# Kernel optimization log

Hardware: AMD Instinct MI355X
Metric: run time of the kernel (lower is better)

The kernel has to match this reference:

```python
import jax, jax.numpy as jnp
import numpy as np

EPS = 1e-12
SHRINK = 0.0025

def _l2norm(x, axis=1):
    return x / jnp.maximum(jnp.linalg.norm(x, axis=axis, keepdims=True), EPS)

def setup_inputs() -> dict:
    key = jax.random.key(0)
    ks = jax.random.split(key, 6)
    N, C, H, W = 32, 512, 32, 32
    mem_dim, spatial = 512, H * W
    hid = spatial // 2
    x = jax.random.normal(ks[0], (N, C, H, W), dtype=jnp.float32)
    memory = jax.random.normal(ks[1], (mem_dim, spatial), dtype=jnp.float32)
    memory = _l2norm(memory, axis=1)  # buffer is L2-normalized at init
    w1 = jax.random.normal(ks[2], (hid, spatial), dtype=jnp.float32) * 0.02
    b1 = jax.random.normal(ks[3], (hid,), dtype=jnp.float32) * 0.02
    w2 = jax.random.normal(ks[4], (spatial, hid), dtype=jnp.float32) * 0.02
    b2 = jax.random.normal(ks[5], (spatial,), dtype=jnp.float32) * 0.02
    return {"x": x, "memory": memory, "w1": w1, "b1": b1, "w2": w2, "b2": b2}

def reference(x, memory, w1, b1, w2, b2):
    N, C, H, W = x.shape
    mem_dim = memory.shape[0]
    input_flat = x.reshape(N * C, H * W)
    input_norm = _l2norm(input_flat, axis=1)
    # shared MLP over memory bank: Linear -> ReLU -> Linear -> ReLU
    h = jax.nn.relu(memory @ w1.T + b1)
    mem_proc = jax.nn.relu(h @ w2.T + b2)
    memory_norm = _l2norm(mem_proc, axis=1)
    # addressing: cosine sim -> softmax -> hard shrink -> L1 renorm
    att = jax.nn.softmax(input_norm @ memory_norm.T, axis=1)  # [N*C, M]
    att = jax.nn.relu(att - SHRINK)
    att = att / jnp.maximum(att.sum(axis=1, keepdims=True), EPS)  # p=1 norm (att >= 0)
    output = (att @ memory_norm).reshape(N, C, H, W)
    att_channel_avg = att.reshape(N, C, mem_dim).mean(axis=1)  # [N, M]
    att_spatial = jnp.broadcast_to(att_channel_avg[:, :, None, None], (N, mem_dim, H, W))
    return output, att_spatial, input_flat, memory_norm, att
```

## Files before the change

### kernel.cpp

```cpp
#include <hip/hip_runtime.h>

typedef float  f32x4  __attribute__((ext_vector_type(4)));
typedef __bf16 bf16x8 __attribute__((ext_vector_type(8)));
typedef __bf16 bf16x4 __attribute__((ext_vector_type(4)));

#define L2EPS   1e-12f
#define SHRINKC 0.0025f


__device__ __forceinline__ bf16x8 pack_bf16(f32x4 v0, f32x4 v1) {
  bf16x8 r;
  r[0] = (__bf16)v0[0]; r[1] = (__bf16)v0[1]; r[2] = (__bf16)v0[2]; r[3] = (__bf16)v0[3];
  r[4] = (__bf16)v1[0]; r[5] = (__bf16)v1[1]; r[6] = (__bf16)v1[2]; r[7] = (__bf16)v1[3];
  return r;
}

__device__ __forceinline__ bf16x8 load_cvt_bf16x8(const float* p) {
  const f32x4* q = (const f32x4*)p;
  return pack_bf16(q[0], q[1]);
}

__global__ __launch_bounds__(256) void rownorm_copy(
    const float* __restrict__ x, float* __restrict__ out_flat,
    float* __restrict__ invnorm) {
  const int r = blockIdx.x;
  const int tid = threadIdx.x;
  const f32x4 v = *(const f32x4*)(x + (size_t)r * 1024 + tid * 4);
  *(f32x4*)(out_flat + (size_t)r * 1024 + tid * 4) = v;
  float ss = v[0]*v[0] + v[1]*v[1] + v[2]*v[2] + v[3]*v[3];
  #pragma unroll
  for (int d = 1; d < 64; d <<= 1) ss += __shfl_xor(ss, d);
  __shared__ float wsum[4];
  if ((tid & 63) == 0) wsum[tid >> 6] = ss;
  __syncthreads();
  if (tid == 0) {
    float t = wsum[0] + wsum[1] + wsum[2] + wsum[3];
    invnorm[r] = 1.f / fmaxf(sqrtf(t), L2EPS);
  }
}

__global__ __launch_bounds__(256) void gemm_bt_bias_relu(
    const float* __restrict__ A, const float* __restrict__ B,
    const float* __restrict__ bias, float* __restrict__ C,
    int M, int N, int K) {
  const int r0   = blockIdx.x * 32;
  const int wave = threadIdx.x >> 6;
  const int lane = threadIdx.x & 63;
  const int quad = lane >> 4;
  const int m    = lane & 15;
  const int n0   = blockIdx.y * 128 + wave * 32;

  f32x4 acc[2][2] = {};
  for (int k0 = 0; k0 < K; k0 += 32) {
    const int kk = k0 + quad * 8;
    bf16x8 a[2], b[2];
    #pragma unroll
    for (int rg = 0; rg < 2; ++rg)
      a[rg] = load_cvt_bf16x8(A + (size_t)(r0 + rg * 16 + m) * K + kk);
    #pragma unroll
    for (int cf = 0; cf < 2; ++cf)
      b[cf] = load_cvt_bf16x8(B + (size_t)(n0 + cf * 16 + m) * K + kk);
    #pragma unroll
    for (int rg = 0; rg < 2; ++rg)
      #pragma unroll
      for (int cf = 0; cf < 2; ++cf)
        acc[rg][cf] = __builtin_amdgcn_mfma_f32_16x16x32_bf16(a[rg], b[cf], acc[rg][cf], 0, 0, 0);
  }
  #pragma unroll
  for (int rg = 0; rg < 2; ++rg)
    #pragma unroll
    for (int cf = 0; cf < 2; ++cf) {
      const int n = n0 + cf * 16 + m;
      const float bv = bias[n];
      #pragma unroll
      for (int vi = 0; vi < 4; ++vi) {
        const int r = r0 + rg * 16 + quad * 4 + vi;
        C[(size_t)r * N + n] = fmaxf(acc[rg][cf][vi] + bv, 0.f);
      }
    }
}

__global__ __launch_bounds__(256) void norm_rows(
    const float* __restrict__ mp, float* __restrict__ mn_f32,
    __bf16* __restrict__ mn_bf16) {
  const int r = blockIdx.x;
  const int tid = threadIdx.x;
  const f32x4 v = *(const f32x4*)(mp + (size_t)r * 1024 + tid * 4);
  float ss = v[0]*v[0] + v[1]*v[1] + v[2]*v[2] + v[3]*v[3];
  #pragma unroll
  for (int d = 1; d < 64; d <<= 1) ss += __shfl_xor(ss, d);
  __shared__ float wsum[4];
  __shared__ float invs;
  if ((tid & 63) == 0) wsum[tid >> 6] = ss;
  __syncthreads();
  if (tid == 0) {
    float t = wsum[0] + wsum[1] + wsum[2] + wsum[3];
    invs = 1.f / fmaxf(sqrtf(t), L2EPS);
  }
  __syncthreads();
  const float iv = invs;
  f32x4 o = v * iv;
  *(f32x4*)(mn_f32 + (size_t)r * 1024 + tid * 4) = o;
  bf16x4 ob;
  ob[0] = (__bf16)o[0]; ob[1] = (__bf16)o[1]; ob[2] = (__bf16)o[2]; ob[3] = (__bf16)o[3];
  *(bf16x4*)(mn_bf16 + (size_t)r * 1024 + tid * 4) = ob;
}

__global__ __launch_bounds__(256) void attend(
    const float* __restrict__ x, const float* __restrict__ invnorm,
    const __bf16* __restrict__ Mn, const float* __restrict__ Mnf,
    float* __restrict__ out_out, float* __restrict__ out_att,
    float* __restrict__ attsum) {
  __shared__ float S[32][512];
  const int r0   = blockIdx.x * 32;
  const int tid  = threadIdx.x;
  const int wave = tid >> 6;
  const int lane = tid & 63;
  const int quad = lane >> 4;
  const int m    = lane & 15;
  const int n0w  = wave * 128;

  f32x4 acc[8][2] = {};
  for (int k0 = 0; k0 < 1024; k0 += 32) {
    const int kk = k0 + quad * 8;
    bf16x8 a[2];
    #pragma unroll
    for (int rg = 0; rg < 2; ++rg) {
      const int row = r0 + rg * 16 + m;
      const f32x4* q = (const f32x4*)(x + (size_t)row * 1024 + kk);
      f32x4 v0 = q[0], v1 = q[1];
      const float iv = invnorm[row];
      v0 *= iv; v1 *= iv;
      a[rg] = pack_bf16(v0, v1);
    }
    #pragma unroll
    for (int nf = 0; nf < 8; ++nf) {
      const bf16x8 b = *(const bf16x8*)(Mn + (size_t)(n0w + nf * 16 + m) * 1024 + kk);
      acc[nf][0] = __builtin_amdgcn_mfma_f32_16x16x32_bf16(a[0], b, acc[nf][0], 0, 0, 0);
      acc[nf][1] = __builtin_amdgcn_mfma_f32_16x16x32_bf16(a[1], b, acc[nf][1], 0, 0, 0);
    }
  }
  #pragma unroll
  for (int nf = 0; nf < 8; ++nf)
    #pragma unroll
    for (int rg = 0; rg < 2; ++rg)
      #pragma unroll
      for (int vi = 0; vi < 4; ++vi)
        S[rg * 16 + quad * 4 + vi][n0w + nf * 16 + m] = acc[nf][rg][vi];
  __syncthreads();

  const int row = tid >> 3;
  const int sub = tid & 7;
  float mx = -1e30f;
  for (int i = 0; i < 64; ++i) {
    const int c = (sub + 4 * row + 8 * i) & 511;
    mx = fmaxf(mx, S[row][c]);
  }
  #pragma unroll
  for (int d = 1; d < 8; d <<= 1) mx = fmaxf(mx, __shfl_xor(mx, d));
  float se = 0.f;
  for (int i = 0; i < 64; ++i) {
    const int c = (sub + 4 * row + 8 * i) & 511;
    se += __expf(S[row][c] - mx);
  }
  #pragma unroll
  for (int d = 1; d < 8; d <<= 1) se += __shfl_xor(se, d);
  const float inv_se = 1.f / se;
  float rsum = 0.f;
  for (int i = 0; i < 64; ++i) {
    const int c = (sub + 4 * row + 8 * i) & 511;
    const float sh = fmaxf(__expf(S[row][c] - mx) * inv_se - SHRINKC, 0.f);
    S[row][c] = sh;
    rsum += sh;
  }
  #pragma unroll
  for (int d = 1; d < 8; d <<= 1) rsum += __shfl_xor(rsum, d);
  const float invr = 1.f / fmaxf(rsum, L2EPS);
  for (int i = 0; i < 64; ++i) {
    const int c = (sub + 4 * row + 8 * i) & 511;
    S[row][c] *= invr;
  }
  const int any = __syncthreads_or((sub == 0) && (rsum > 0.f));

  {
    float* dst = out_att + (size_t)r0 * 512;
    for (int idx = tid; idx < 32 * 512 / 4; idx += 256) {
      const int f = idx * 4;
      *(f32x4*)(dst + f) = *(const f32x4*)(&S[f >> 9][f & 511]);
    }
  }

  if (!any) {
    const f32x4 z = {0.f, 0.f, 0.f, 0.f};
    float* dst = out_out + (size_t)r0 * 1024;
    for (int idx = tid; idx < 32 * 1024 / 4; idx += 256)
      *(f32x4*)(dst + idx * 4) = z;
  } else {
    const int nimg = r0 >> 9;
    for (int c = tid; c < 512; c += 256) {
      float s = 0.f;
      for (int rr = 0; rr < 32; ++rr) s += S[rr][c];
      atomicAdd(&attsum[nimg * 512 + c], s);
    }
    const int c0 = tid * 4;
    for (int rr = 0; rr < 32; ++rr) {
      f32x4 o = {0.f, 0.f, 0.f, 0.f};
      for (int mm = 0; mm < 512; ++mm) {
        const float a = S[rr][mm];
        o += a * (*(const f32x4*)(Mnf + (size_t)mm * 1024 + c0));
      }
      *(f32x4*)(out_out + (size_t)(r0 + rr) * 1024 + c0) = o;
    }
  }
}

__global__ __launch_bounds__(256) void spread(
    const float* __restrict__ attsum, float* __restrict__ out_sp) {
  const int nm = blockIdx.x;
  const float v = attsum[nm] * (1.f / 512.f);
  const f32x4 vv = {v, v, v, v};
  *(f32x4*)(out_sp + (size_t)nm * 1024 + threadIdx.x * 4) = vv;
}


extern "C" void kernel_launch(void* const* d_in, const int* in_sizes, int n_in,
                              void* d_out, int out_size, void* d_ws, size_t ws_size,
                              hipStream_t stream) {
  const float* x      = (const float*)d_in[0];
  const float* memory = (const float*)d_in[1];
  const float* w1     = (const float*)d_in[2];
  const float* b1     = (const float*)d_in[3];
  const float* w2     = (const float*)d_in[4];
  const float* b2     = (const float*)d_in[5];

  float* out = (float*)d_out;
  float* out_output = out;
  float* out_attsp  = out + 16777216;
  float* out_flat   = out + 33554432;
  float* out_mnorm  = out + 50331648;
  float* out_att    = out + 50855936;

  char* ws = (char*)d_ws;
  float*  invnorm = (float*)ws;
  float*  h       = (float*)(ws + (1 << 16));
  float*  mp      = (float*)(ws + (1 << 16) + (1 << 20));
  __bf16* mnb     = (__bf16*)(ws + (1 << 16) + (1 << 20) + (2 << 20));
  float*  attsum  = (float*)(ws + (1 << 16) + (1 << 20) + (2 << 20) + (1 << 20));

  hipMemsetAsync(attsum, 0, 32 * 512 * sizeof(float), stream);

  rownorm_copy<<<16384, 256, 0, stream>>>(x, out_flat, invnorm);
  gemm_bt_bias_relu<<<dim3(16, 4), 256, 0, stream>>>(memory, w1, b1, h, 512, 512, 1024);
  gemm_bt_bias_relu<<<dim3(16, 8), 256, 0, stream>>>(h, w2, b2, mp, 512, 1024, 512);
  norm_rows<<<512, 256, 0, stream>>>(mp, out_mnorm, mnb);
  attend<<<512, 256, 0, stream>>>(x, invnorm, mnb, out_mnorm, out_output, out_att, attsum);
  spread<<<16384, 256, 0, stream>>>(attsum, out_attsp);
}
```

Baseline: 428.1 us.

## Fuse input row-norm and flat copy into attend; apply norm post-GEMM

Removes the separate rownorm_copy kernel. The attend kernel now accumulates each row's sum of squares while loading x, writes the flat copy from wave 0, and multiplies the raw dot products by the inverse norm inside the softmax exponent. This relies on softmax being invariant to the max shift under positive scaling. It saves one full read of x plus a kernel launch, at the cost of feeding unnormalized x to the bf16 MFMA. The small MLP GEMMs are also relaunched with 64-thread blocks over more blocks to spread them across more CUs.

```diff
diff --git a/kernel.cpp b/kernel.cpp
--- a/kernel.cpp
+++ b/kernel.cpp
@@ -20,35 +20,19 @@
   return pack_bf16(q[0], q[1]);
 }
 
-__global__ __launch_bounds__(256) void rownorm_copy(
-    const float* __restrict__ x, float* __restrict__ out_flat,
-    float* __restrict__ invnorm) {
-  const int r = blockIdx.x;
-  const int tid = threadIdx.x;
-  const f32x4 v = *(const f32x4*)(x + (size_t)r * 1024 + tid * 4);
-  *(f32x4*)(out_flat + (size_t)r * 1024 + tid * 4) = v;
-  float ss = v[0]*v[0] + v[1]*v[1] + v[2]*v[2] + v[3]*v[3];
-  #pragma unroll
-  for (int d = 1; d < 64; d <<= 1) ss += __shfl_xor(ss, d);
-  __shared__ float wsum[4];
-  if ((tid & 63) == 0) wsum[tid >> 6] = ss;
-  __syncthreads();
-  if (tid == 0) {
-    float t = wsum[0] + wsum[1] + wsum[2] + wsum[3];
-    invnorm[r] = 1.f / fmaxf(sqrtf(t), L2EPS);
-  }
-}
-
-__global__ __launch_bounds__(256) void gemm_bt_bias_relu(
+__device__ __forceinline__ float dot4(f32x4 v) {
+  return v[0]*v[0] + v[1]*v[1] + v[2]*v[2] + v[3]*v[3];
+}
+
+__global__ __launch_bounds__(64) void gemm_bt_bias_relu(
     const float* __restrict__ A, const float* __restrict__ B,
     const float* __restrict__ bias, float* __restrict__ C,
     int M, int N, int K) {
   const int r0   = blockIdx.x * 32;
-  const int wave = threadIdx.x >> 6;
+  const int n0   = blockIdx.y * 32;
   const int lane = threadIdx.x & 63;
   const int quad = lane >> 4;
   const int m    = lane & 15;
-  const int n0   = blockIdx.y * 128 + wave * 32;
 
   f32x4 acc[2][2] = {};
   for (int k0 = 0; k0 < K; k0 += 32) {
@@ -86,7 +70,7 @@
   const int r = blockIdx.x;
   const int tid = threadIdx.x;
   const f32x4 v = *(const f32x4*)(mp + (size_t)r * 1024 + tid * 4);
-  float ss = v[0]*v[0] + v[1]*v[1] + v[2]*v[2] + v[3]*v[3];
+  float ss = dot4(v);
   #pragma unroll
   for (int d = 1; d < 64; d <<= 1) ss += __shfl_xor(ss, d);
   __shared__ float wsum[4];
@@ -107,11 +91,12 @@
 }
 
 __global__ __launch_bounds__(256) void attend(
-    const float* __restrict__ x, const float* __restrict__ invnorm,
-    const __bf16* __restrict__ Mn, const float* __restrict__ Mnf,
+    const float* __restrict__ x, const __bf16* __restrict__ Mn,
+    const float* __restrict__ Mnf, float* __restrict__ out_flat,
     float* __restrict__ out_out, float* __restrict__ out_att,
     float* __restrict__ attsum) {
   __shared__ float S[32][512];
+  __shared__ float invn[32];
   const int r0   = blockIdx.x * 32;
   const int tid  = threadIdx.x;
   const int wave = tid >> 6;
@@ -120,18 +105,31 @@
   const int m    = lane & 15;
   const int n0w  = wave * 128;
 
+  float ss0 = 0.f, ss1 = 0.f;
   f32x4 acc[8][2] = {};
   for (int k0 = 0; k0 < 1024; k0 += 32) {
     const int kk = k0 + quad * 8;
     bf16x8 a[2];
-    #pragma unroll
-    for (int rg = 0; rg < 2; ++rg) {
-      const int row = r0 + rg * 16 + m;
+    f32x4 v0a, v0b, v1a, v1b;
+    {
+      const int row = r0 + m;
       const f32x4* q = (const f32x4*)(x + (size_t)row * 1024 + kk);
-      f32x4 v0 = q[0], v1 = q[1];
-      const float iv = invnorm[row];
-      v0 *= iv; v1 *= iv;
-      a[rg] = pack_bf16(v0, v1);
+      v0a = q[0]; v0b = q[1];
+      a[0] = pack_bf16(v0a, v0b);
+      ss0 += dot4(v0a) + dot4(v0b);
+    }
+    {
+      const int row = r0 + 16 + m;
+      const f32x4* q = (const f32x4*)(x + (size_t)row * 1024 + kk);
+      v1a = q[0]; v1b = q[1];
+      a[1] = pack_bf16(v1a, v1b);
+      ss1 += dot4(v1a) + dot4(v1b);
+    }
+    if (wave == 0) {
+      float* d0 = out_flat + (size_t)(r0 + m) * 1024 + kk;
+      float* d1 = out_flat + (size_t)(r0 + 16 + m) * 1024 + kk;
+      *(f32x4*)d0 = v0a; *(f32x4*)(d0 + 4) = v0b;
+      *(f32x4*)d1 = v1a; *(f32x4*)(d1 + 4) = v1b;
     }
     #pragma unroll
     for (int nf = 0; nf < 8; ++nf) {
@@ -139,6 +137,12 @@
       acc[nf][0] = __builtin_amdgcn_mfma_f32_16x16x32_bf16(a[0], b, acc[nf][0], 0, 0, 0);
       acc[nf][1] = __builtin_amdgcn_mfma_f32_16x16x32_bf16(a[1], b, acc[nf][1], 0, 0, 0);
     }
+  }
+  ss0 += __shfl_xor(ss0, 16); ss0 += __shfl_xor(ss0, 32);
+  ss1 += __shfl_xor(ss1, 16); ss1 += __shfl_xor(ss1, 32);
+  if (wave == 0 && quad == 0) {
+    invn[m]      = 1.f / fmaxf(sqrtf(ss0), L2EPS);
+    invn[16 + m] = 1.f / fmaxf(sqrtf(ss1), L2EPS);
   }
   #pragma unroll
   for (int nf = 0; nf < 8; ++nf)
@@ -151,6 +155,7 @@
 
   const int row = tid >> 3;
   const int sub = tid & 7;
+  const float iv = invn[row];
   float mx = -1e30f;
   for (int i = 0; i < 64; ++i) {
     const int c = (sub + 4 * row + 8 * i) & 511;
@@ -161,7 +166,7 @@
   float se = 0.f;
   for (int i = 0; i < 64; ++i) {
     const int c = (sub + 4 * row + 8 * i) & 511;
-    se += __expf(S[row][c] - mx);
+    se += __expf((S[row][c] - mx) * iv);
   }
   #pragma unroll
   for (int d = 1; d < 8; d <<= 1) se += __shfl_xor(se, d);
@@ -169,7 +174,7 @@
   float rsum = 0.f;
   for (int i = 0; i < 64; ++i) {
     const int c = (sub + 4 * row + 8 * i) & 511;
-    const float sh = fmaxf(__expf(S[row][c] - mx) * inv_se - SHRINKC, 0.f);
+    const float sh = fmaxf(__expf((S[row][c] - mx) * iv) * inv_se - SHRINKC, 0.f);
     S[row][c] = sh;
     rsum += sh;
   }
@@ -241,18 +246,16 @@
   float* out_att    = out + 50855936;
 
   char* ws = (char*)d_ws;
-  float*  invnorm = (float*)ws;
-  float*  h       = (float*)(ws + (1 << 16));
-  float*  mp      = (float*)(ws + (1 << 16) + (1 << 20));
-  __bf16* mnb     = (__bf16*)(ws + (1 << 16) + (1 << 20) + (2 << 20));
-  float*  attsum  = (float*)(ws + (1 << 16) + (1 << 20) + (2 << 20) + (1 << 20));
+  float*  h      = (float*)ws;
+  float*  mp     = (float*)(ws + (1 << 20));
+  __bf16* mnb    = (__bf16*)(ws + (1 << 20) + (2 << 20));
+  float*  attsum = (float*)(ws + (1 << 20) + (2 << 20) + (1 << 20));
 
   hipMemsetAsync(attsum, 0, 32 * 512 * sizeof(float), stream);
 
-  rownorm_copy<<<16384, 256, 0, stream>>>(x, out_flat, invnorm);
-  gemm_bt_bias_relu<<<dim3(16, 4), 256, 0, stream>>>(memory, w1, b1, h, 512, 512, 1024);
-  gemm_bt_bias_relu<<<dim3(16, 8), 256, 0, stream>>>(h, w2, b2, mp, 512, 1024, 512);
+  gemm_bt_bias_relu<<<dim3(16, 16), 64, 0, stream>>>(memory, w1, b1, h, 512, 512, 1024);
+  gemm_bt_bias_relu<<<dim3(16, 32), 64, 0, stream>>>(h, w2, b2, mp, 512, 1024, 512);
   norm_rows<<<512, 256, 0, stream>>>(mp, out_mnorm, mnb);
-  attend<<<512, 256, 0, stream>>>(x, invnorm, mnb, out_mnorm, out_output, out_att, attsum);
+  attend<<<512, 256, 0, stream>>>(x, mnb, out_mnorm, out_flat, out_output, out_att, attsum);
   spread<<<16384, 256, 0, stream>>>(attsum, out_attsp);
 }
```

Result: faster. 419.3 us (-2.1%).
